# Performance work log

Hardware: AMD Instinct MI355X
Metric: run time of the kernel (lower is better)

Reference implementation:

```python
import jax, jax.numpy as jnp
import numpy as np

N_NODES = 100000


def setup_inputs() -> dict:
    key = jax.random.key(0)
    k1, k2, k3, k4, k5 = jax.random.split(key, 5)
    feat = jax.random.normal(k1, (N_NODES, 256), dtype=jnp.float32)
    w_neigh = jax.random.normal(k2, (128, 256), dtype=jnp.float32) * (1.0 / np.sqrt(256))
    bias = jax.random.normal(k3, (128,), dtype=jnp.float32) * 0.01
    src = jax.random.randint(k4, (1600000,), 0, N_NODES, dtype=jnp.int64)
    dst = jax.random.randint(k5, (1600000,), 0, N_NODES, dtype=jnp.int64)
    return {"feat": feat, "w_neigh": w_neigh, "bias": bias, "src": src, "dst": dst}


def reference(feat, w_neigh, bias, src, dst):
    # pass_type='low', aggregator='mean', lin_before_mp (in_feats 256 > out_feats 128)
    n = feat.shape[0]
    h = feat @ w_neigh.T                              # [N, out] fc_neigh before MP
    msg = h[src]                                      # gather  [E, out]
    agg = jax.ops.segment_sum(msg, dst, num_segments=n)   # scatter-sum [N, out]
    deg = jax.ops.segment_sum(jnp.ones_like(dst, dtype=h.dtype), dst, num_segments=n)
    neigh = agg / jnp.maximum(deg, 1.0)[:, None]      # mean; zero-degree nodes -> 0 (DGL semantics)
    return neigh + bias
```

## Files before the change

kernel.cpp:

```cpp
#include <hip/hip_runtime.h>
#include <hip/hip_bf16.h>

typedef __attribute__((ext_vector_type(8))) short short8;
typedef __attribute__((ext_vector_type(4))) float floatx4;

#define F_IN 256
#define F_OUT 128
#define NODE_SHIFT 8
#define BKT_NODES 256
#define MAX_BKT 2048
#define AGG_THREADS 512
#define AGG_CAP 6144
#define FILL_BLOCKS 128
#define FILL_THREADS 512
#define GEMM_THREADS 256

static __device__ __forceinline__ short f32_to_bf16_bits(float v) {
    __hip_bfloat16 t = __float2bfloat16(v);
    return *reinterpret_cast<short*>(&t);
}
static __device__ __forceinline__ float bf16bits_to_f32(unsigned short u) {
    unsigned x = (unsigned)u << 16;
    return __builtin_bit_cast(float, x);
}

__global__ __launch_bounds__(256) void detect_kernel(
    const void* __restrict__ featp, const void* __restrict__ dstp,
    int* __restrict__ flags, int* __restrict__ bucket_counts, int nbkt)
{
    for (int j = threadIdx.x; j < nbkt; j += 256) bucket_counts[j] = 0;
    if (threadIdx.x == 0) {
        const unsigned short* fb = (const unsigned short*)featp;
        int plaus = 0;
        for (int i = 0; i < 64; ++i) {
            unsigned short u = fb[2 * i];
            int ex = (u >> 7) & 0xFF;
            if (ex >= 118 && ex <= 137) plaus++;
        }
        flags[0] = (plaus >= 48) ? 0 : 1;

        const int* di = (const int*)dstp;
        int zeros = 0;
        for (int i = 0; i < 64; ++i)
            if (di[2 * i + 1] == 0) zeros++;
        flags[1] = (zeros >= 62) ? 1 : 0;
        flags[8] = 0;
    }
}

__global__ __launch_bounds__(256) void bincount_scan_kernel(
    const void* __restrict__ dstp, int* __restrict__ bucket_counts,
    int* __restrict__ offsets, int* __restrict__ cursor,
    int n_edges, int n_nodes, int nbkt, int* __restrict__ flags)
{
    const int i64 = flags[1];
    __shared__ int hist[MAX_BKT];
    __shared__ int is_last;
    const bool use_lds = (nbkt <= MAX_BKT);
    if (use_lds) {
        for (int j = threadIdx.x; j < nbkt; j += 256) hist[j] = 0;
        __syncthreads();
    }
    const int stride = gridDim.x * blockDim.x;
    for (int e = blockIdx.x * blockDim.x + threadIdx.x; e < n_edges; e += stride) {
        int d = i64 ? (int)((const long long*)dstp)[e] : ((const int*)dstp)[e];
        if ((unsigned)d >= (unsigned)n_nodes) continue;
        if (use_lds) atomicAdd(&hist[d >> NODE_SHIFT], 1);
        else         atomicAdd(&bucket_counts[d >> NODE_SHIFT], 1);
    }
    if (use_lds) {
        __syncthreads();
        for (int j = threadIdx.x; j < nbkt; j += 256) {
            int c = hist[j];
            if (c) atomicAdd(&bucket_counts[j], c);
        }
    }
    __threadfence();
    if (threadIdx.x == 0)
        is_last = (atomicAdd(&flags[8], 1) == (int)gridDim.x - 1);
    __syncthreads();
    if (!is_last) return;

    const int t = threadIdx.x;
    const int base = t * 16;
    int v[16];
    int run = 0;
#pragma unroll
    for (int j = 0; j < 16; ++j) {
        int idx = base + j;
        int x = (idx < nbkt)
            ? __hip_atomic_load(&bucket_counts[idx], __ATOMIC_RELAXED,
                                __HIP_MEMORY_SCOPE_AGENT)
            : 0;
        v[j] = run;
        run += x;
    }
    __syncthreads();
    hist[t] = run;
    __syncthreads();
    for (int off = 1; off < 256; off <<= 1) {
        int x = (t >= off) ? hist[t - off] : 0;
        __syncthreads();
        hist[t] += x;
        __syncthreads();
    }
    const int excl = hist[t] - run;
#pragma unroll
    for (int j = 0; j < 16; ++j) {
        int idx = base + j;
        if (idx < nbkt) {
            int o = excl + v[j];
            offsets[idx] = o;
            cursor[idx]  = o;
        }
    }
}

__global__ __launch_bounds__(GEMM_THREADS) void gemm_kernel(
    const void* __restrict__ featp, const void* __restrict__ wp,
    unsigned short* __restrict__ hp, int n_nodes, int n_tiles,
    const int* __restrict__ flags)
{
    __shared__ short8 wfrag[4096];
    const int f32mode = flags[0];

    for (int d = threadIdx.x; d < 4096; d += GEMM_THREADS) {
        const int nt   = d >> 9;
        const int ks   = (d >> 6) & 7;
        const int kg   = (d >> 4) & 3;
        const int mrow = d & 15;
        const int row  = nt * 16 + mrow;
        const int c    = row * 32 + ks * 4 + kg;
        short8 v;
        if (!f32mode) {
            v = *(const short8*)((const char*)wp + (c << 4));
        } else {
            const float* f = (const float*)wp + c * 8;
            floatx4 v0 = *(const floatx4*)f;
            floatx4 v1 = *(const floatx4*)(f + 4);
#pragma unroll
            for (int j = 0; j < 4; ++j) {
                v[j]     = f32_to_bf16_bits(v0[j]);
                v[4 + j] = f32_to_bf16_bits(v1[j]);
            }
        }
        wfrag[d] = v;
    }
    __syncthreads();

    const int wid  = threadIdx.x >> 6;
    const int lane = threadIdx.x & 63;
    const int mrow = lane & 15;
    const int kg   = lane >> 4;

    auto loadA = [&](int tile, short8 (&a)[8]) {
        const int lrow = min(tile * 64 + wid * 16 + mrow, n_nodes - 1);
        if (!f32mode) {
            const short* fr = (const short*)featp + (size_t)lrow * F_IN;
#pragma unroll
            for (int ks = 0; ks < 8; ++ks)
                a[ks] = *(const short8*)(fr + ks * 32 + kg * 8);
        } else {
            const float* fr = (const float*)featp + (size_t)lrow * F_IN;
#pragma unroll
            for (int ks = 0; ks < 8; ++ks) {
                floatx4 v0 = *(const floatx4*)(fr + ks * 32 + kg * 8);
                floatx4 v1 = *(const floatx4*)(fr + ks * 32 + kg * 8 + 4);
                short8 t;
#pragma unroll
                for (int j = 0; j < 4; ++j) {
                    t[j]     = f32_to_bf16_bits(v0[j]);
                    t[4 + j] = f32_to_bf16_bits(v1[j]);
                }
                a[ks] = t;
            }
        }
    };

    auto compute = [&](int tile, short8 (&a)[8]) {
        floatx4 acc[8];
#pragma unroll
        for (int nt = 0; nt < 8; ++nt) acc[nt] = (floatx4){0.f, 0.f, 0.f, 0.f};
#pragma unroll
        for (int nt = 0; nt < 8; ++nt) {
#pragma unroll
            for (int ks = 0; ks < 8; ++ks) {
                const short8 b = wfrag[((nt * 8 + ks) << 6) + lane];
                acc[nt] = __builtin_amdgcn_mfma_f32_16x16x32_bf16(a[ks], b, acc[nt], 0, 0, 0);
            }
        }
        const int m0 = tile * 64 + wid * 16;
#pragma unroll
        for (int nt = 0; nt < 8; ++nt) {
            const int col = nt * 16 + mrow;
#pragma unroll
            for (int r = 0; r < 4; ++r) {
                const int orow = m0 + kg * 4 + r;
                if (orow < n_nodes)
                    hp[(size_t)orow * F_OUT + col] = (unsigned short)f32_to_bf16_bits(acc[nt][r]);
            }
        }
    };

    int tile = blockIdx.x;
    if (tile >= n_tiles) return;
    short8 a0[8], a1[8];
    loadA(tile, a0);
    bool cur0 = true;
    for (; tile < n_tiles; tile += gridDim.x) {
        const int nxt = tile + gridDim.x;
        if (cur0) {
            if (nxt < n_tiles) loadA(nxt, a1);
            compute(tile, a0);
        } else {
            if (nxt < n_tiles) loadA(nxt, a0);
            compute(tile, a1);
        }
        cur0 = !cur0;
    }
}

__global__ __launch_bounds__(FILL_THREADS) void binfill_kernel(
    const void* __restrict__ srcp, const void* __restrict__ dstp,
    int* __restrict__ cursor, unsigned* __restrict__ bucket_edges,
    int n_edges, int n_nodes, int nbkt, const int* __restrict__ flags)
{
    const int i64 = flags[1];
    __shared__ int hist[MAX_BKT];
    __shared__ int base[MAX_BKT];

    if (nbkt > MAX_BKT) {
        const int stride = gridDim.x * blockDim.x;
        for (int e = blockIdx.x * blockDim.x + threadIdx.x; e < n_edges; e += stride) {
            int s, d;
            if (i64) { s = (int)((const long long*)srcp)[e]; d = (int)((const long long*)dstp)[e]; }
            else     { s = ((const int*)srcp)[e];            d = ((const int*)dstp)[e]; }
            if ((unsigned)d >= (unsigned)n_nodes) continue;
            if ((unsigned)s >= (unsigned)n_nodes) s = 0;
            int pos = atomicAdd(&cursor[d >> NODE_SHIFT], 1);
            bucket_edges[pos] = (unsigned)s | ((unsigned)(d & (BKT_NODES - 1)) << 24);
        }
        return;
    }

    const int chunk = (n_edges + gridDim.x - 1) / gridDim.x;
    const int e0 = blockIdx.x * chunk;
    const int e1 = min(e0 + chunk, n_edges);

    for (int j = threadIdx.x; j < nbkt; j += FILL_THREADS) hist[j] = 0;
    __syncthreads();
    for (int e = e0 + threadIdx.x; e < e1; e += FILL_THREADS) {
        int d = i64 ? (int)((const long long*)dstp)[e] : ((const int*)dstp)[e];
        if ((unsigned)d < (unsigned)n_nodes) atomicAdd(&hist[d >> NODE_SHIFT], 1);
    }
    __syncthreads();
    for (int j = threadIdx.x; j < nbkt; j += FILL_THREADS) {
        int c = hist[j];
        base[j] = c ? atomicAdd(&cursor[j], c) : 0;
    }
    __syncthreads();
    for (int j = threadIdx.x; j < nbkt; j += FILL_THREADS) hist[j] = 0;
    __syncthreads();
    for (int e = e0 + threadIdx.x; e < e1; e += FILL_THREADS) {
        int s, d;
        if (i64) { s = (int)((const long long*)srcp)[e]; d = (int)((const long long*)dstp)[e]; }
        else     { s = ((const int*)srcp)[e];            d = ((const int*)dstp)[e]; }
        if ((unsigned)d >= (unsigned)n_nodes) continue;
        if ((unsigned)s >= (unsigned)n_nodes) s = 0;
        const int b = d >> NODE_SHIFT;
        int pos = base[b] + atomicAdd(&hist[b], 1);
        bucket_edges[pos] = (unsigned)s | ((unsigned)(d & (BKT_NODES - 1)) << 24);
    }
}

__global__ __launch_bounds__(AGG_THREADS) void agg_kernel(
    const unsigned short* __restrict__ h, const unsigned* __restrict__ bucket_edges,
    const int* __restrict__ bucket_offsets, const int* __restrict__ bucket_counts,
    const void* __restrict__ biasp, void* __restrict__ outp,
    int n_nodes, int nbkt, const int* __restrict__ flags)
{
    __shared__ int s_src[AGG_CAP];
    __shared__ int hist[BKT_NODES];
    __shared__ int excl[BKT_NODES];
    __shared__ int cur2[BKT_NODES];
    __shared__ int node_cursor;

    const int f32mode = flags[0];
    const int tid = threadIdx.x;
    const int wave = tid >> 6;
    const int lane = tid & 63;
    const int grp  = lane >> 4;
    const int sub  = lane & 15;

    float bs[8];
    if (f32mode) {
#pragma unroll
        for (int j = 0; j < 8; ++j) bs[j] = ((const float*)biasp)[sub * 8 + j];
    } else {
#pragma unroll
        for (int j = 0; j < 8; ++j)
            bs[j] = bf16bits_to_f32(((const unsigned short*)biasp)[sub * 8 + j]);
    }

    for (int bkt = blockIdx.x; bkt < nbkt; bkt += gridDim.x) {
        const int beg = bucket_offsets[bkt];
        const int cnt = bucket_counts[bkt];
        const int node0 = bkt << NODE_SHIFT;

        if (cnt > AGG_CAP) {
            float bx, by;
            if (f32mode) {
                bx = ((const float*)biasp)[lane * 2];
                by = ((const float*)biasp)[lane * 2 + 1];
            } else {
                bx = bf16bits_to_f32(((const unsigned short*)biasp)[lane * 2]);
                by = bf16bits_to_f32(((const unsigned short*)biasp)[lane * 2 + 1]);
            }
            for (int nl = wave; nl < BKT_NODES; nl += AGG_THREADS / 64) {
                const int node = node0 + nl;
                if (node >= n_nodes) continue;
                float ax = 0.f, ay = 0.f;
                int deg = 0;
                for (int i = 0; i < cnt; ++i) {
                    const unsigned pk = bucket_edges[beg + i];
                    if ((int)(pk >> 24) == nl) {
                        const int s = (int)(pk & 0xFFFFFF);
                        unsigned p = *(const unsigned*)(h + (size_t)s * F_OUT + lane * 2);
                        ax += bf16bits_to_f32((unsigned short)p);
                        ay += bf16bits_to_f32((unsigned short)(p >> 16));
                        deg++;
                    }
                }
                const float scale = 1.0f / fmaxf((float)deg, 1.0f);
                float ox = ax * scale + bx, oy = ay * scale + by;
                if (f32mode) {
                    ((float*)outp)[(size_t)node * F_OUT + lane * 2]     = ox;
                    ((float*)outp)[(size_t)node * F_OUT + lane * 2 + 1] = oy;
                } else {
                    unsigned pkv = ((unsigned)(unsigned short)f32_to_bf16_bits(oy) << 16) |
                                   (unsigned)(unsigned short)f32_to_bf16_bits(ox);
                    ((unsigned*)outp)[(size_t)node * (F_OUT / 2) + lane] = pkv;
                }
            }
            continue;
        }

        __syncthreads();

        if (tid < BKT_NODES) hist[tid] = 0;
        if (tid == 0) node_cursor = 0;
        __syncthreads();
        for (int i = tid; i < cnt; i += AGG_THREADS)
            atomicAdd(&hist[bucket_edges[beg + i] >> 24], 1);
        __syncthreads();
        if (wave == 0) {
            const int b0 = lane * 4;
            const int h0 = hist[b0], h1 = hist[b0 + 1],
                      h2 = hist[b0 + 2], h3 = hist[b0 + 3];
            const int lsum = h0 + h1 + h2 + h3;
            int run = lsum;
#pragma unroll
            for (int off = 1; off < 64; off <<= 1) {
                int x = __shfl_up(run, off);
                if (lane >= off) run += x;
            }
            const int lexcl = run - lsum;
            excl[b0]     = lexcl;                cur2[b0]     = lexcl;
            excl[b0 + 1] = lexcl + h0;           cur2[b0 + 1] = lexcl + h0;
            excl[b0 + 2] = lexcl + h0 + h1;      cur2[b0 + 2] = lexcl + h0 + h1;
            excl[b0 + 3] = lexcl + h0 + h1 + h2; cur2[b0 + 3] = lexcl + h0 + h1 + h2;
        }
        __syncthreads();
        for (int i = tid; i < cnt; i += AGG_THREADS) {
            const unsigned pk = bucket_edges[beg + i];
            const int pos = atomicAdd(&cur2[pk >> 24], 1);
            s_src[pos] = (int)(pk & 0xFFFFFF);
        }
        __syncthreads();

        for (;;) {
            int nl;
            if (lane == 0) nl = atomicAdd(&node_cursor, 1);
            nl = __shfl(nl, 0);
            if (nl >= BKT_NODES) break;
            const int node = node0 + nl;
            if (node >= n_nodes) continue;

            const int nbeg = excl[nl];
            const int ncnt = hist[nl];

            float acc[8];
#pragma unroll
            for (int j = 0; j < 8; ++j) acc[j] = 0.f;

            int i = 0;
            for (; i + 15 < ncnt; i += 16) {
                const int s0 = s_src[nbeg + i + grp];
                const int s1 = s_src[nbeg + i + 4 + grp];
                const int s2 = s_src[nbeg + i + 8 + grp];
                const int s3 = s_src[nbeg + i + 12 + grp];
                const short8 v0 = *(const short8*)(h + (size_t)s0 * F_OUT + sub * 8);
                const short8 v1 = *(const short8*)(h + (size_t)s1 * F_OUT + sub * 8);
                const short8 v2 = *(const short8*)(h + (size_t)s2 * F_OUT + sub * 8);
                const short8 v3 = *(const short8*)(h + (size_t)s3 * F_OUT + sub * 8);
#pragma unroll
                for (int j = 0; j < 8; ++j) {
                    acc[j] += bf16bits_to_f32((unsigned short)v0[j]);
                    acc[j] += bf16bits_to_f32((unsigned short)v1[j]);
                    acc[j] += bf16bits_to_f32((unsigned short)v2[j]);
                    acc[j] += bf16bits_to_f32((unsigned short)v3[j]);
                }
            }
            for (; i + 7 < ncnt; i += 8) {
                const int s0 = s_src[nbeg + i + grp];
                const int s1 = s_src[nbeg + i + 4 + grp];
                const short8 v0 = *(const short8*)(h + (size_t)s0 * F_OUT + sub * 8);
                const short8 v1 = *(const short8*)(h + (size_t)s1 * F_OUT + sub * 8);
#pragma unroll
                for (int j = 0; j < 8; ++j) {
                    acc[j] += bf16bits_to_f32((unsigned short)v0[j]);
                    acc[j] += bf16bits_to_f32((unsigned short)v1[j]);
                }
            }
            for (; i < ncnt; i += 4) {
                const int e = i + grp;
                if (e < ncnt) {
                    const int s = s_src[nbeg + e];
                    const short8 v = *(const short8*)(h + (size_t)s * F_OUT + sub * 8);
#pragma unroll
                    for (int j = 0; j < 8; ++j)
                        acc[j] += bf16bits_to_f32((unsigned short)v[j]);
                }
            }

#pragma unroll
            for (int j = 0; j < 8; ++j) {
                acc[j] += __shfl_xor(acc[j], 16);
                acc[j] += __shfl_xor(acc[j], 32);
            }

            const float scale = 1.0f / fmaxf((float)ncnt, 1.0f);
            if (lane < 16) {
                if (f32mode) {
                    float* o = (float*)outp + (size_t)node * F_OUT + sub * 8;
                    floatx4 o0, o1;
#pragma unroll
                    for (int j = 0; j < 4; ++j) {
                        o0[j] = acc[j] * scale + bs[j];
                        o1[j] = acc[4 + j] * scale + bs[4 + j];
                    }
                    *(floatx4*)o = o0;
                    *(floatx4*)(o + 4) = o1;
                } else {
                    short8 r;
#pragma unroll
                    for (int j = 0; j < 8; ++j)
                        r[j] = f32_to_bf16_bits(acc[j] * scale + bs[j]);
                    *(short8*)((unsigned short*)outp + (size_t)node * F_OUT + sub * 8) = r;
                }
            }
        }
    }
}

extern "C" void kernel_launch(void* const* d_in, const int* in_sizes, int n_in,
                              void* d_out, int out_size, void* d_ws, size_t ws_size,
                              hipStream_t stream)
{
    const void* feat = d_in[0];
    const void* w    = d_in[1];
    const void* bias = d_in[2];
    const void* src  = d_in[3];
    const void* dst  = d_in[4];
    const int n_nodes = in_sizes[0] / F_IN;
    const int n_edges = in_sizes[3];
    const int nbkt = (n_nodes + BKT_NODES - 1) / BKT_NODES;

    char* ws = (char*)d_ws;
    auto align256 = [](size_t x) { return (x + 255) & ~(size_t)255; };

    size_t off = 0;
    int* flags = (int*)(ws + off);              off = align256(off + 256);
    int* bucket_counts = (int*)(ws + off);      off = align256(off + (size_t)nbkt * 4);
    int* bucket_offsets = (int*)(ws + off);     off = align256(off + (size_t)nbkt * 4);
    int* cursor = (int*)(ws + off);             off = align256(off + (size_t)nbkt * 4);
    unsigned* bucket_edges = (unsigned*)(ws + off);
    off = align256(off + (size_t)n_edges * 4);
    unsigned short* hp = (unsigned short*)(ws + off);
    off = align256(off + (size_t)n_nodes * F_OUT * 2);

    detect_kernel<<<1, 256, 0, stream>>>(feat, dst, flags, bucket_counts, nbkt);

    bincount_scan_kernel<<<256, 256, 0, stream>>>(dst, bucket_counts,
                                                  bucket_offsets, cursor,
                                                  n_edges, n_nodes, nbkt, flags);

    const int n_tiles = (n_nodes + 63) / 64;
    const int gemm_blocks = min(512, n_tiles);
    gemm_kernel<<<gemm_blocks, GEMM_THREADS, 0, stream>>>(
        feat, w, hp, n_nodes, n_tiles, flags);

    binfill_kernel<<<FILL_BLOCKS, FILL_THREADS, 0, stream>>>(
        src, dst, cursor, bucket_edges, n_edges, n_nodes, nbkt, flags);

    const int agg_blocks = min(1024, nbkt);
    agg_kernel<<<agg_blocks, AGG_THREADS, 0, stream>>>(
        hp, bucket_edges, bucket_offsets, bucket_counts, bias, d_out,
        n_nodes, nbkt, flags);
}
```

Baseline: 162.4 us.

## Replace bincount+scan with fixed-capacity per-bucket edge slots

Removes the separate bucket histogram and prefix-scan kernel. Each bucket now gets a fixed-capacity region (about twice the average edge count) and binfill appends into it using the cursor as both count and position. Buckets that overflow the capacity fall back to a slow path in the aggregation kernel that rescans all edges. This saves one full pass over dst and one launch, at the cost of a larger workspace and a pathological path for skewed graphs.

```diff
diff --git a/kernel.cpp b/kernel.cpp
--- a/kernel.cpp
+++ b/kernel.cpp
@@ -26,9 +26,9 @@
 
 __global__ __launch_bounds__(256) void detect_kernel(
     const void* __restrict__ featp, const void* __restrict__ dstp,
-    int* __restrict__ flags, int* __restrict__ bucket_counts, int nbkt)
+    int* __restrict__ flags, int* __restrict__ cursor, int nbkt)
 {
-    for (int j = threadIdx.x; j < nbkt; j += 256) bucket_counts[j] = 0;
+    for (int j = threadIdx.x; j < nbkt; j += 256) cursor[j] = 0;
     if (threadIdx.x == 0) {
         const unsigned short* fb = (const unsigned short*)featp;
         int plaus = 0;
@@ -44,75 +44,6 @@
         for (int i = 0; i < 64; ++i)
             if (di[2 * i + 1] == 0) zeros++;
         flags[1] = (zeros >= 62) ? 1 : 0;
-        flags[8] = 0;
-    }
-}
-
-__global__ __launch_bounds__(256) void bincount_scan_kernel(
-    const void* __restrict__ dstp, int* __restrict__ bucket_counts,
-    int* __restrict__ offsets, int* __restrict__ cursor,
-    int n_edges, int n_nodes, int nbkt, int* __restrict__ flags)
-{
-    const int i64 = flags[1];
-    __shared__ int hist[MAX_BKT];
-    __shared__ int is_last;
-    const bool use_lds = (nbkt <= MAX_BKT);
-    if (use_lds) {
-        for (int j = threadIdx.x; j < nbkt; j += 256) hist[j] = 0;
-        __syncthreads();
-    }
-    const int stride = gridDim.x * blockDim.x;
-    for (int e = blockIdx.x * blockDim.x + threadIdx.x; e < n_edges; e += stride) {
-        int d = i64 ? (int)((const long long*)dstp)[e] : ((const int*)dstp)[e];
-        if ((unsigned)d >= (unsigned)n_nodes) continue;
-        if (use_lds) atomicAdd(&hist[d >> NODE_SHIFT], 1);
-        else         atomicAdd(&bucket_counts[d >> NODE_SHIFT], 1);
-    }
-    if (use_lds) {
-        __syncthreads();
-        for (int j = threadIdx.x; j < nbkt; j += 256) {
-            int c = hist[j];
-            if (c) atomicAdd(&bucket_counts[j], c);
-        }
-    }
-    __threadfence();
-    if (threadIdx.x == 0)
-        is_last = (atomicAdd(&flags[8], 1) == (int)gridDim.x - 1);
-    __syncthreads();
-    if (!is_last) return;
-
-    const int t = threadIdx.x;
-    const int base = t * 16;
-    int v[16];
-    int run = 0;
-#pragma unroll
-    for (int j = 0; j < 16; ++j) {
-        int idx = base + j;
-        int x = (idx < nbkt)
-            ? __hip_atomic_load(&bucket_counts[idx], __ATOMIC_RELAXED,
-                                __HIP_MEMORY_SCOPE_AGENT)
-            : 0;
-        v[j] = run;
-        run += x;
-    }
-    __syncthreads();
-    hist[t] = run;
-    __syncthreads();
-    for (int off = 1; off < 256; off <<= 1) {
-        int x = (t >= off) ? hist[t - off] : 0;
-        __syncthreads();
-        hist[t] += x;
-        __syncthreads();
-    }
-    const int excl = hist[t] - run;
-#pragma unroll
-    for (int j = 0; j < 16; ++j) {
-        int idx = base + j;
-        if (idx < nbkt) {
-            int o = excl + v[j];
-            offsets[idx] = o;
-            cursor[idx]  = o;
-        }
     }
 }
 
@@ -223,7 +154,7 @@
 __global__ __launch_bounds__(FILL_THREADS) void binfill_kernel(
     const void* __restrict__ srcp, const void* __restrict__ dstp,
     int* __restrict__ cursor, unsigned* __restrict__ bucket_edges,
-    int n_edges, int n_nodes, int nbkt, const int* __restrict__ flags)
+    int n_edges, int n_nodes, int nbkt, int cap, const int* __restrict__ flags)
 {
     const int i64 = flags[1];
     __shared__ int hist[MAX_BKT];
@@ -237,8 +168,11 @@
             else     { s = ((const int*)srcp)[e];            d = ((const int*)dstp)[e]; }
             if ((unsigned)d >= (unsigned)n_nodes) continue;
             if ((unsigned)s >= (unsigned)n_nodes) s = 0;
-            int pos = atomicAdd(&cursor[d >> NODE_SHIFT], 1);
-            bucket_edges[pos] = (unsigned)s | ((unsigned)(d & (BKT_NODES - 1)) << 24);
+            const int b = d >> NODE_SHIFT;
+            int pos = atomicAdd(&cursor[b], 1);
+            if (pos < cap)
+                bucket_edges[(size_t)b * cap + pos] =
+                    (unsigned)s | ((unsigned)(d & (BKT_NODES - 1)) << 24);
         }
         return;
     }
@@ -268,16 +202,19 @@
         if ((unsigned)d >= (unsigned)n_nodes) continue;
         if ((unsigned)s >= (unsigned)n_nodes) s = 0;
         const int b = d >> NODE_SHIFT;
-        int pos = base[b] + atomicAdd(&hist[b], 1);
-        bucket_edges[pos] = (unsigned)s | ((unsigned)(d & (BKT_NODES - 1)) << 24);
+        const int pos = base[b] + atomicAdd(&hist[b], 1);
+        if (pos < cap)
+            bucket_edges[(size_t)b * cap + pos] =
+                (unsigned)s | ((unsigned)(d & (BKT_NODES - 1)) << 24);
     }
 }
 
 __global__ __launch_bounds__(AGG_THREADS) void agg_kernel(
     const unsigned short* __restrict__ h, const unsigned* __restrict__ bucket_edges,
-    const int* __restrict__ bucket_offsets, const int* __restrict__ bucket_counts,
+    const int* __restrict__ cursor, const void* __restrict__ srcp,
+    const void* __restrict__ dstp, int n_edges,
     const void* __restrict__ biasp, void* __restrict__ outp,
-    int n_nodes, int nbkt, const int* __restrict__ flags)
+    int n_nodes, int nbkt, int cap, const int* __restrict__ flags)
 {
     __shared__ int s_src[AGG_CAP];
     __shared__ int hist[BKT_NODES];
@@ -286,6 +223,7 @@
     __shared__ int node_cursor;
 
     const int f32mode = flags[0];
+    const int i64 = flags[1];
     const int tid = threadIdx.x;
     const int wave = tid >> 6;
     const int lane = tid & 63;
@@ -303,9 +241,50 @@
     }
 
     for (int bkt = blockIdx.x; bkt < nbkt; bkt += gridDim.x) {
-        const int beg = bucket_offsets[bkt];
-        const int cnt = bucket_counts[bkt];
+        const size_t beg = (size_t)bkt * cap;
+        const int cnt = cursor[bkt];
         const int node0 = bkt << NODE_SHIFT;
+
+        if (cnt > cap) {
+            float bx, by;
+            if (f32mode) {
+                bx = ((const float*)biasp)[lane * 2];
+                by = ((const float*)biasp)[lane * 2 + 1];
+            } else {
+                bx = bf16bits_to_f32(((const unsigned short*)biasp)[lane * 2]);
+                by = bf16bits_to_f32(((const unsigned short*)biasp)[lane * 2 + 1]);
+            }
+            for (int nl = wave; nl < BKT_NODES; nl += AGG_THREADS / 64) {
+                const int node = node0 + nl;
+                if (node >= n_nodes) continue;
+                float ax = 0.f, ay = 0.f;
+                int deg = 0;
+                for (int e = 0; e < n_edges; ++e) {
+                    int d = i64 ? (int)((const long long*)dstp)[e]
+                                : ((const int*)dstp)[e];
+                    if (d == node) {
+                        int s = i64 ? (int)((const long long*)srcp)[e]
+                                    : ((const int*)srcp)[e];
+                        if ((unsigned)s >= (unsigned)n_nodes) s = 0;
+                        unsigned p = *(const unsigned*)(h + (size_t)s * F_OUT + lane * 2);
+                        ax += bf16bits_to_f32((unsigned short)p);
+                        ay += bf16bits_to_f32((unsigned short)(p >> 16));
+                        deg++;
+                    }
+                }
+                const float scale = 1.0f / fmaxf((float)deg, 1.0f);
+                float ox = ax * scale + bx, oy = ay * scale + by;
+                if (f32mode) {
+                    ((float*)outp)[(size_t)node * F_OUT + lane * 2]     = ox;
+                    ((float*)outp)[(size_t)node * F_OUT + lane * 2 + 1] = oy;
+                } else {
+                    unsigned pkv = ((unsigned)(unsigned short)f32_to_bf16_bits(oy) << 16) |
+                                   (unsigned)(unsigned short)f32_to_bf16_bits(ox);
+                    ((unsigned*)outp)[(size_t)node * (F_OUT / 2) + lane] = pkv;
+                }
+            }
+            continue;
+        }
 
         if (cnt > AGG_CAP) {
             float bx, by;
@@ -476,24 +455,21 @@
     const int n_edges = in_sizes[3];
     const int nbkt = (n_nodes + BKT_NODES - 1) / BKT_NODES;
 
+    int cap = (int)((2LL * n_edges / nbkt + 1023) / 1024) * 1024;
+    if (cap < 2048) cap = 2048;
+
     char* ws = (char*)d_ws;
     auto align256 = [](size_t x) { return (x + 255) & ~(size_t)255; };
 
     size_t off = 0;
     int* flags = (int*)(ws + off);              off = align256(off + 256);
-    int* bucket_counts = (int*)(ws + off);      off = align256(off + (size_t)nbkt * 4);
-    int* bucket_offsets = (int*)(ws + off);     off = align256(off + (size_t)nbkt * 4);
     int* cursor = (int*)(ws + off);             off = align256(off + (size_t)nbkt * 4);
     unsigned* bucket_edges = (unsigned*)(ws + off);
-    off = align256(off + (size_t)n_edges * 4);
+    off = align256(off + (size_t)nbkt * cap * 4);
     unsigned short* hp = (unsigned short*)(ws + off);
     off = align256(off + (size_t)n_nodes * F_OUT * 2);
 
-    detect_kernel<<<1, 256, 0, stream>>>(feat, dst, flags, bucket_counts, nbkt);
-
-    bincount_scan_kernel<<<256, 256, 0, stream>>>(dst, bucket_counts,
-                                                  bucket_offsets, cursor,
-                                                  n_edges, n_nodes, nbkt, flags);
+    detect_kernel<<<1, 256, 0, stream>>>(feat, dst, flags, cursor, nbkt);
 
     const int n_tiles = (n_nodes + 63) / 64;
     const int gemm_blocks = min(512, n_tiles);
@@ -501,10 +477,10 @@
         feat, w, hp, n_nodes, n_tiles, flags);
 
     binfill_kernel<<<FILL_BLOCKS, FILL_THREADS, 0, stream>>>(
-        src, dst, cursor, bucket_edges, n_edges, n_nodes, nbkt, flags);
+        src, dst, cursor, bucket_edges, n_edges, n_nodes, nbkt, cap, flags);
 
     const int agg_blocks = min(1024, nbkt);
     agg_kernel<<<agg_blocks, AGG_THREADS, 0, stream>>>(
-        hp, bucket_edges, bucket_offsets, bucket_counts, bias, d_out,
-        n_nodes, nbkt, flags);
-}
+        hp, bucket_edges, cursor, src, dst, n_edges, bias, d_out,
+        n_nodes, nbkt, cap, flags);
+}
```

Measured after the change: 136.0 us. 16.2% less time.
